# Kernel tuning notes

Hardware: AMD Instinct MI355X
Metric: run time of the kernel (lower is better)

Reference implementation:

```python
import jax, jax.numpy as jnp
import numpy as np

B, N = 1, 1024
C_A, C_Z, H = 768, 128, 16
CH = C_A // H  # 48
INV_SQRT_CH = float(1.0 / np.sqrt(CH))


def _ln(x, w, b):
    # torch.nn.LayerNorm over last dim, eps=1e-5
    m = jnp.mean(x, axis=-1, keepdims=True)
    v = jnp.mean(jnp.square(x - m), axis=-1, keepdims=True)
    return (x - m) * jax.lax.rsqrt(v + 1e-5) * w + b


def setup_inputs() -> dict:
    key = jax.random.key(0)
    ks = jax.random.split(key, 8)
    rn = lambda k, shape, sc: jax.random.normal(k, shape, dtype=jnp.float32) * sc
    return {
        "a": rn(ks[0], (B, N, C_A), 1.0),
        "z": rn(ks[1], (B, N, N, C_Z), 1.0),
        "mask": jnp.ones((B, N), dtype=jnp.float32),
        "ln_a_w": jnp.ones((C_A,), jnp.float32),
        "ln_a_b": jnp.zeros((C_A,), jnp.float32),
        "ln_z_w": jnp.ones((C_Z,), jnp.float32),
        "ln_z_b": jnp.zeros((C_Z,), jnp.float32),
        "Wq": rn(ks[2], (C_A, H * CH), 0.02),
        "bq": jnp.zeros((H * CH,), jnp.float32),
        "Wk": rn(ks[3], (C_A, H * CH), 0.02),
        "Wv": rn(ks[4], (C_A, H * CH), 0.02),
        "Wb": rn(ks[5], (C_Z, H), 0.02),
        "Wg": rn(ks[6], (C_A, H * CH), 0.02),
        "Wo": rn(ks[7], (H * CH, C_A), 0.02),
    }


def reference(a, z, mask, ln_a_w, ln_a_b, ln_z_w, ln_z_b, Wq, bq, Wk, Wv, Wb, Wg, Wo):
    an = _ln(a, ln_a_w, ln_a_b)                                  # [B, N, C_A]
    q = (an @ Wq + bq).reshape(B, N, H, CH)
    k = (an @ Wk).reshape(B, N, H, CH)
    v = (an @ Wv).reshape(B, N, H, CH)
    # pair bias: LayerNorm(z) -> per-head scalar bias [B, N, N, H]
    bpair = _ln(z, ln_z_w, ln_z_b) @ Wb
    mbias = (mask - 1.0)[:, None, None, :] * 1e9                  # [B, 1, 1, N]
    logits = jnp.einsum('bqhc,bkhc->bhqk', q, k) * INV_SQRT_CH
    logits = logits + jnp.transpose(bpair, (0, 3, 1, 2)) + mbias  # [B, H, N, N]
    attn = jax.nn.softmax(logits, axis=-1)
    o = jnp.einsum('bhqk,bkhc->bqhc', attn, v)                    # [B, N, H, CH]
    g = jax.nn.sigmoid(an @ Wg).reshape(B, N, H, CH)
    out = (g * o).reshape(B, N, H * CH) @ Wo                      # [B, N, C_A]
    return out
```

## Files before the change

### kernel.cpp

```cpp
#include <hip/hip_runtime.h>

#define NSEQ 1024
#define CA   768
#define CZ   128
#define NH   16
#define CHD  48
#define HC   768
#define INV_SQRT_CH 0.14433756729740643f

typedef float v4f __attribute__((ext_vector_type(4)));
typedef short v8s __attribute__((ext_vector_type(8)));

__device__ __forceinline__ short f2bf(float f) {
  union { float f; unsigned u; } v; v.f = f;
  unsigned r = v.u + 0x7fffu + ((v.u >> 16) & 1u);
  return (short)(r >> 16);
}
__device__ __forceinline__ float bf2f(short s) {
  union { unsigned u; float f; } v;
  v.u = ((unsigned)(unsigned short)s) << 16;
  return v.f;
}
__device__ __forceinline__ unsigned cvtpk(float lo, float hi) {
  unsigned r;
  asm("v_cvt_pk_bf16_f32 %0, %1, %2" : "=v"(r) : "v"(lo), "v"(hi));
  return r;
}

__global__ __launch_bounds__(256) void k_front(
    const float* __restrict__ lnzw, const float* __restrict__ lnzb,
    const float* __restrict__ Wb, short* __restrict__ wWp, float* __restrict__ S1bW,
    const float* __restrict__ Wq, const float* __restrict__ Wk,
    const float* __restrict__ Wv, const float* __restrict__ Wg,
    const float* __restrict__ Wo, short* __restrict__ WT, short* __restrict__ WoT,
    const float* __restrict__ a, const float* __restrict__ lnaw,
    const float* __restrict__ lnab, short* __restrict__ anb)
{
  __shared__ __align__(16) char fsm[64 * 65 * 4];
  const int bid = blockIdx.x;
  const int t = threadIdx.x;

  if (bid == 0) {
    const int s = t >> 6, l = t & 63;
    const int r16 = l & 15, cg = l >> 4;
    float v[8];
    #pragma unroll
    for (int j = 0; j < 8; ++j) {
      int d = s * 32 + cg * 8 + j;
      v[j] = lnzw[d] * Wb[d * NH + r16];
    }
    uint4 pk;
    pk.x = cvtpk(v[0], v[1]); pk.y = cvtpk(v[2], v[3]);
    pk.z = cvtpk(v[4], v[5]); pk.w = cvtpk(v[6], v[7]);
    *(uint4*)(wWp + (s * 64 + l) * 8) = pk;
    if (t < NH) {
      float s1 = 0.f, bw = 0.f;
      for (int d = 0; d < CZ; ++d) {
        float wb = Wb[d * NH + t];
        s1 += bf2f(f2bf(lnzw[d] * wb));
        bw += lnzb[d] * wb;
      }
      S1bW[t] = s1;
      S1bW[NH + t] = bw;
    }
  } else if (bid <= 720) {
    float (*tile)[65] = (float(*)[65])fsm;
    const int cb = bid - 1;
    const int mat = cb / 144, rem = cb % 144;
    const int tk = rem % 12, tn = rem / 12;
    const int k0 = tk * 64, n0 = tn * 64;
    const float* __restrict__ W =
        (mat == 0) ? Wq : (mat == 1) ? Wk : (mat == 2) ? Wv : (mat == 3) ? Wg : Wo;
    const float s = (mat == 0) ? INV_SQRT_CH : 1.f;
    const int rr = t >> 4, cc = (t & 15) * 4;
    #pragma unroll
    for (int r = 0; r < 4; ++r) {
      v4f v = *(const v4f*)(W + (size_t)(k0 + r * 16 + rr) * HC + n0 + cc);
      tile[r * 16 + rr][cc + 0] = v[0];
      tile[r * 16 + rr][cc + 1] = v[1];
      tile[r * 16 + rr][cc + 2] = v[2];
      tile[r * 16 + rr][cc + 3] = v[3];
    }
    __syncthreads();
    short* dst = (mat < 4) ? (WT + (size_t)mat * HC * CA) : WoT;
    #pragma unroll
    for (int r = 0; r < 4; ++r) {
      const int nr = r * 16 + rr;
      uint2 pk;
      pk.x = cvtpk(tile[cc + 0][nr] * s, tile[cc + 1][nr] * s);
      pk.y = cvtpk(tile[cc + 2][nr] * s, tile[cc + 3][nr] * s);
      *(uint2*)(dst + (size_t)(n0 + nr) * CA + k0 + cc) = pk;
    }
  } else {
    float* red = (float*)fsm;
    const int row = bid - 721;
    const float* ar = a + (size_t)row * CA;
    float x[3];
    float s = 0.f, s2 = 0.f;
    #pragma unroll
    for (int i = 0; i < 3; ++i) {
      x[i] = ar[t + i * 256];
      s += x[i]; s2 += x[i] * x[i];
    }
    #pragma unroll
    for (int off = 1; off < 64; off <<= 1) {
      s += __shfl_xor(s, off);
      s2 += __shfl_xor(s2, off);
    }
    const int wv = t >> 6;
    if ((t & 63) == 0) { red[wv] = s; red[4 + wv] = s2; }
    __syncthreads();
    s = red[0] + red[1] + red[2] + red[3];
    s2 = red[4] + red[5] + red[6] + red[7];
    const float m = s * (1.f / CA);
    const float var = s2 * (1.f / CA) - m * m;
    const float rs = rsqrtf(var + 1e-5f);
    #pragma unroll
    for (int i = 0; i < 3; ++i) {
      int c = t + i * 256;
      anb[(size_t)row * CA + c] = f2bf((x[i] - m) * rs * lnaw[c] + lnab[c]);
    }
  }
}

__global__ __launch_bounds__(256) void k23_mega(
    const short* __restrict__ anb, const short* __restrict__ WT,
    const float* __restrict__ bq, const float* __restrict__ z,
    const short* __restrict__ wWp, const float* __restrict__ S1bW,
    short* __restrict__ qb, short* __restrict__ kb, short* __restrict__ vT,
    float* __restrict__ gbuf, short* __restrict__ bpair)
{
  __shared__ __align__(16) char smem[20480];
  const int tid = threadIdx.x;
  const int w = tid >> 6, l = tid & 63;
  const int r16 = l & 15, cg = l >> 4;

  if (blockIdx.x < 192) {
    short* As = (short*)smem;
    short* Bs = (short*)(smem + 10240);
    const int bm = blockIdx.x & 7;
    const int bnb = blockIdx.x >> 3;
    const int m0 = bm * 128, n0 = bnb * 128;
    const int wr = w >> 1, wc = w & 1;
    const int strow = w * 16 + (l >> 2);
    const int scol = (l & 3) * 8;

    v4f acc[4][4];
    #pragma unroll
    for (int i = 0; i < 4; ++i)
      #pragma unroll
      for (int j = 0; j < 4; ++j)
        acc[i][j] = (v4f){0.f, 0.f, 0.f, 0.f};

    for (int k0 = 0; k0 < CA; k0 += 32) {
      v8s av0 = *(const v8s*)(anb + (size_t)(m0 + strow) * CA + k0 + scol);
      v8s av1 = *(const v8s*)(anb + (size_t)(m0 + 64 + strow) * CA + k0 + scol);
      v8s bv0 = *(const v8s*)(WT + (size_t)(n0 + strow) * CA + k0 + scol);
      v8s bv1 = *(const v8s*)(WT + (size_t)(n0 + 64 + strow) * CA + k0 + scol);
      __syncthreads();
      *(v8s*)(As + (size_t)strow * 40 + scol) = av0;
      *(v8s*)(As + (size_t)(64 + strow) * 40 + scol) = av1;
      *(v8s*)(Bs + (size_t)strow * 40 + scol) = bv0;
      *(v8s*)(Bs + (size_t)(64 + strow) * 40 + scol) = bv1;
      __syncthreads();
      v8s a[4], b[4];
      #pragma unroll
      for (int m = 0; m < 4; ++m)
        a[m] = *(const v8s*)(As + (wr * 64 + m * 16 + r16) * 40 + cg * 8);
      #pragma unroll
      for (int n = 0; n < 4; ++n)
        b[n] = *(const v8s*)(Bs + (wc * 64 + n * 16 + r16) * 40 + cg * 8);
      #pragma unroll
      for (int m = 0; m < 4; ++m)
        #pragma unroll
        for (int n = 0; n < 4; ++n)
          acc[m][n] = __builtin_amdgcn_mfma_f32_16x16x32_bf16(a[m], b[n], acc[m][n], 0, 0, 0);
    }

    const int matsel = n0 / HC;
    #pragma unroll
    for (int n = 0; n < 4; ++n) {
      const int nc = (n0 % HC) + wc * 64 + n * 16 + r16;
      const int rbase = m0 + wr * 64 + cg * 4;
      if (matsel == 0) {
        const float bqs = bq[nc] * INV_SQRT_CH;
        #pragma unroll
        for (int m = 0; m < 4; ++m)
          #pragma unroll
          for (int j = 0; j < 4; ++j)
            qb[(size_t)(rbase + m * 16 + j) * HC + nc] = f2bf(acc[m][n][j] + bqs);
      } else if (matsel == 1) {
        #pragma unroll
        for (int m = 0; m < 4; ++m)
          #pragma unroll
          for (int j = 0; j < 4; ++j)
            kb[(size_t)(rbase + m * 16 + j) * HC + nc] = f2bf(acc[m][n][j]);
      } else if (matsel == 2) {
        #pragma unroll
        for (int m = 0; m < 4; ++m) {
          uint2 pk;
          pk.x = cvtpk(acc[m][n][0], acc[m][n][1]);
          pk.y = cvtpk(acc[m][n][2], acc[m][n][3]);
          *(uint2*)(vT + (size_t)nc * NSEQ + rbase + m * 16) = pk;
        }
      } else {
        #pragma unroll
        for (int m = 0; m < 4; ++m)
          #pragma unroll
          for (int j = 0; j < 4; ++j)
            gbuf[(size_t)(rbase + m * 16 + j) * HC + nc] =
                1.f / (1.f + __expf(-acc[m][n][j]));
      }
    }
  } else {
    const int zbid = blockIdx.x - 192;
    short* bl = (short*)smem + w * (16 * 68);
    const int q = zbid >> 2;
    const int kw = ((zbid & 3) << 8) + w * 64;

    v8s bfrag[4];
    #pragma unroll
    for (int s = 0; s < 4; ++s) bfrag[s] = *(const v8s*)(wWp + (s * 64 + l) * 8);
    const float S1 = S1bW[r16];
    const float bW = S1bW[NH + r16];

    const float* __restrict__ zbase = z + ((size_t)q * NSEQ + kw + r16) * CZ;

    v4f zb[8];
    #pragma unroll
    for (int s = 0; s < 4; ++s) {
      zb[2 * s]     = *(const v4f*)(zbase + s * 32 + cg * 8);
      zb[2 * s + 1] = *(const v4f*)(zbase + s * 32 + cg * 8 + 4);
    }

    for (int kt = 0; kt < 4; ++kt) {
      v4f zn[8];
      if (kt < 3) {
        const float* __restrict__ zr2 = zbase + (size_t)(kt + 1) * 16 * CZ;
        #pragma unroll
        for (int s = 0; s < 4; ++s) {
          zn[2 * s]     = *(const v4f*)(zr2 + s * 32 + cg * 8);
          zn[2 * s + 1] = *(const v4f*)(zr2 + s * 32 + cg * 8 + 4);
        }
      }

      float sum = 0.f, sum2 = 0.f;
      v8s afrag[4];
      #pragma unroll
      for (int s = 0; s < 4; ++s) {
        v4f z0 = zb[2 * s], z1 = zb[2 * s + 1];
        #pragma unroll
        for (int j = 0; j < 4; ++j) {
          sum += z0[j] + z1[j];
          sum2 += z0[j] * z0[j] + z1[j] * z1[j];
        }
        union { v8s s8; unsigned u[4]; } fu;
        fu.u[0] = cvtpk(z0[0], z0[1]);
        fu.u[1] = cvtpk(z0[2], z0[3]);
        fu.u[2] = cvtpk(z1[0], z1[1]);
        fu.u[3] = cvtpk(z1[2], z1[3]);
        afrag[s] = fu.s8;
      }
      sum  += __shfl_xor(sum, 16);  sum  += __shfl_xor(sum, 32);
      sum2 += __shfl_xor(sum2, 16); sum2 += __shfl_xor(sum2, 32);
      const float mean = sum * (1.f / CZ);
      const float var = sum2 * (1.f / CZ) - mean * mean;
      const float rs = rsqrtf(var + 1e-5f);

      v4f acc = {0.f, 0.f, 0.f, 0.f};
      #pragma unroll
      for (int s = 0; s < 4; ++s)
        acc = __builtin_amdgcn_mfma_f32_16x16x32_bf16(afrag[s], bfrag[s], acc, 0, 0, 0);

      float bv[4];
      #pragma unroll
      for (int j = 0; j < 4; ++j) {
        int src = cg * 4 + j;
        float mj = __shfl(mean, src);
        float rj = __shfl(rs, src);
        bv[j] = rj * (acc[j] - mj * S1) + bW;
      }
      *(unsigned*)&bl[r16 * 68 + kt * 16 + cg * 4]     = cvtpk(bv[0], bv[1]);
      *(unsigned*)&bl[r16 * 68 + kt * 16 + cg * 4 + 2] = cvtpk(bv[2], bv[3]);

      if (kt < 3) {
        #pragma unroll
        for (int i = 0; i < 8; ++i) zb[i] = zn[i];
      }
    }

    asm volatile("s_waitcnt lgkmcnt(0)" ::: "memory");
    __builtin_amdgcn_sched_barrier(0);

    const int h = l >> 2, ck = (l & 3) * 16;
    v8s o0 = *(const v8s*)(bl + h * 68 + ck);
    v8s o1 = *(const v8s*)(bl + h * 68 + ck + 8);
    short* dst = bpair + (size_t)h * NSEQ * NSEQ + (size_t)q * NSEQ + kw + ck;
    *(v8s*)(dst)     = o0;
    *(v8s*)(dst + 8) = o1;
  }
}

#define PL_STRIDE 136
#define PO_STRIDE 52
__global__ __launch_bounds__(512) void k45_attn(
    const short* __restrict__ qb, const short* __restrict__ kb,
    const short* __restrict__ vT, const short* __restrict__ bpair,
    const float* __restrict__ mask, const float* __restrict__ gbuf,
    short* __restrict__ gob)
{
  const int h = blockIdx.x & 15;
  const int qt = blockIdx.x >> 4;
  const int tid = threadIdx.x;
  const int w = tid >> 6, l = tid & 63;
  const int r16 = l & 15, cg = l >> 4;
  const int q0 = qt * 16;
  const int k0 = w * 128;

  __shared__ __align__(16) short plds[8][16 * PL_STRIDE];
  __shared__ __align__(16) float po_lds[8][16][PO_STRIDE];
  __shared__ __align__(16) float ml_lds[8][16][2];
  short* pl = &plds[w][0];

  const v8s vzero = {0, 0, 0, 0, 0, 0, 0, 0};
  v8s qf0, qf1;
  {
    const short* qp = qb + (size_t)(q0 + r16) * HC + h * CHD;
    qf0 = *(const v8s*)(qp + cg * 8);
    qf1 = (cg < 2) ? *(const v8s*)(qp + 32 + cg * 8) : vzero;
  }

  const size_t bpb = (size_t)h * NSEQ * NSEQ;
  {
    const int srow = l >> 2;
    const int scol = (l & 3) * 32;
    const short* bsrc = bpair + bpb + (size_t)(q0 + srow) * NSEQ + k0 + scol;
    short* bdst = pl + srow * PL_STRIDE + scol;
    v8s t0 = *(const v8s*)(bsrc);
    v8s t1 = *(const v8s*)(bsrc + 8);
    v8s t2 = *(const v8s*)(bsrc + 16);
    v8s t3 = *(const v8s*)(bsrc + 24);
    *(v8s*)(bdst)      = t0;
    *(v8s*)(bdst + 8)  = t1;
    *(v8s*)(bdst + 16) = t2;
    *(v8s*)(bdst + 24) = t3;
  }

  v4f cs[8];
  #pragma unroll
  for (int kt = 0; kt < 8; ++kt) {
    const short* kp = kb + (size_t)(k0 + kt * 16 + r16) * HC + h * CHD;
    v8s b0 = *(const v8s*)(kp + cg * 8);
    v8s b1 = (cg < 2) ? *(const v8s*)(kp + 32 + cg * 8) : vzero;
    v4f tacc = {0.f, 0.f, 0.f, 0.f};
    tacc = __builtin_amdgcn_mfma_f32_16x16x32_bf16(qf0, b0, tacc, 0, 0, 0);
    tacc = __builtin_amdgcn_mfma_f32_16x16x32_bf16(qf1, b1, tacc, 0, 0, 0);
    cs[kt] = tacc;
  }

  #pragma unroll
  for (int kt = 0; kt < 8; ++kt) {
    const int kc = k0 + kt * 16 + r16;
    const float mb = (mask[kc] - 1.f) * 1e9f;
    #pragma unroll
    for (int j = 0; j < 4; ++j)
      cs[kt][j] += bf2f(pl[(cg * 4 + j) * PL_STRIDE + kt * 16 + r16]) + mb;
  }

  float mx4[4], ls4[4];
  #pragma unroll
  for (int j = 0; j < 4; ++j) {
    float mx = fmaxf(fmaxf(fmaxf(cs[0][j], cs[1][j]), fmaxf(cs[2][j], cs[3][j])),
                     fmaxf(fmaxf(cs[4][j], cs[5][j]), fmaxf(cs[6][j], cs[7][j])));
    mx = fmaxf(mx, __shfl_xor(mx, 1));
    mx = fmaxf(mx, __shfl_xor(mx, 2));
    mx = fmaxf(mx, __shfl_xor(mx, 4));
    mx = fmaxf(mx, __shfl_xor(mx, 8));
    mx4[j] = mx;
    float p[8];
    #pragma unroll
    for (int kt = 0; kt < 8; ++kt) p[kt] = __expf(cs[kt][j] - mx);
    float rsum = ((p[0] + p[1]) + (p[2] + p[3])) + ((p[4] + p[5]) + (p[6] + p[7]));
    rsum += __shfl_xor(rsum, 1);
    rsum += __shfl_xor(rsum, 2);
    rsum += __shfl_xor(rsum, 4);
    rsum += __shfl_xor(rsum, 8);
    ls4[j] = rsum;
    const int rowb = (cg * 4 + j) * PL_STRIDE;
    #pragma unroll
    for (int t2 = 0; t2 < 4; ++t2) {
      unsigned u = cvtpk(p[2 * t2], p[2 * t2 + 1]);
      pl[rowb + (2 * t2) * 16 + r16] = (short)u;
      pl[rowb + (2 * t2 + 1) * 16 + r16] = (short)(u >> 16);
    }
  }
  asm volatile("s_waitcnt lgkmcnt(0)" ::: "memory");
  __builtin_amdgcn_sched_barrier(0);

  v4f of0 = {0, 0, 0, 0}, of1 = {0, 0, 0, 0}, of2 = {0, 0, 0, 0};
  #pragma unroll
  for (int ks4 = 0; ks4 < 4; ++ks4) {
    v8s pa = *(const v8s*)(pl + r16 * PL_STRIDE + ks4 * 32 + cg * 8);
    const short* vp = vT + (size_t)(h * CHD + r16) * NSEQ + k0 + ks4 * 32 + cg * 8;
    v8s bv0 = *(const v8s*)vp;
    v8s bv1 = *(const v8s*)(vp + 16 * NSEQ);
    v8s bv2 = *(const v8s*)(vp + 32 * NSEQ);
    of0 = __builtin_amdgcn_mfma_f32_16x16x32_bf16(pa, bv0, of0, 0, 0, 0);
    of1 = __builtin_amdgcn_mfma_f32_16x16x32_bf16(pa, bv1, of1, 0, 0, 0);
    of2 = __builtin_amdgcn_mfma_f32_16x16x32_bf16(pa, bv2, of2, 0, 0, 0);
  }

  #pragma unroll
  for (int j = 0; j < 4; ++j) {
    const int row = cg * 4 + j;
    po_lds[w][row][r16]      = of0[j];
    po_lds[w][row][16 + r16] = of1[j];
    po_lds[w][row][32 + r16] = of2[j];
    if (r16 == 0) {
      ml_lds[w][row][0] = mx4[j];
      ml_lds[w][row][1] = ls4[j];
    }
  }
  __syncthreads();

  {
    const int g = tid >> 5;
    const int lane = tid & 31;
    float mi[8], li[8];
    #pragma unroll
    for (int i = 0; i < 8; ++i) {
      mi[i] = ml_lds[i][g][0];
      li[i] = ml_lds[i][g][1];
    }
    float mstar = -1e30f;
    #pragma unroll
    for (int i = 0; i < 8; ++i) mstar = fmaxf(mstar, mi[i]);
    float wgt[8], L = 0.f;
    #pragma unroll
    for (int i = 0; i < 8; ++i) { wgt[i] = __expf(mi[i] - mstar); L += li[i] * wgt[i]; }
    const float inv = 1.f / L;
    const int q = q0 + g;
    {
      float o = 0.f;
      #pragma unroll
      for (int i = 0; i < 8; ++i) o += po_lds[i][g][lane] * wgt[i];
      const float gv = gbuf[(size_t)q * HC + h * CHD + lane];
      gob[(size_t)q * HC + h * CHD + lane] = f2bf(o * inv * gv);
    }
    if (lane < 16) {
      const int d = 32 + lane;
      float o = 0.f;
      #pragma unroll
      for (int i = 0; i < 8; ++i) o += po_lds[i][g][d] * wgt[i];
      const float gv = gbuf[(size_t)q * HC + h * CHD + d];
      gob[(size_t)q * HC + h * CHD + d] = f2bf(o * inv * gv);
    }
  }
}

__global__ __launch_bounds__(256) void k5_out(
    const short* __restrict__ gob, const short* __restrict__ WoT,
    float* __restrict__ out)
{
  __shared__ __align__(16) short As[64 * 40];
  __shared__ __align__(16) short Bs[64 * 40];
  const int tid = threadIdx.x;
  const int w = tid >> 6, l = tid & 63;
  const int r16 = l & 15, cg = l >> 4;
  const int bm = blockIdx.x & 15;
  const int bn = blockIdx.x >> 4;
  const int m0 = bm * 64, n0 = bn * 64;
  const int wr = w >> 1, wc = w & 1;
  const int strow = tid >> 2;
  const int scol = (tid & 3) * 8;

  v4f acc[2][2];
  #pragma unroll
  for (int i = 0; i < 2; ++i)
    #pragma unroll
    for (int j = 0; j < 2; ++j)
      acc[i][j] = (v4f){0.f, 0.f, 0.f, 0.f};

  for (int k0 = 0; k0 < CA; k0 += 32) {
    v8s av = *(const v8s*)(gob + (size_t)(m0 + strow) * CA + k0 + scol);
    v8s bv = *(const v8s*)(WoT + (size_t)(n0 + strow) * CA + k0 + scol);
    __syncthreads();
    *(v8s*)(As + (size_t)strow * 40 + scol) = av;
    *(v8s*)(Bs + (size_t)strow * 40 + scol) = bv;
    __syncthreads();
    v8s a[2], b[2];
    #pragma unroll
    for (int m = 0; m < 2; ++m)
      a[m] = *(const v8s*)(As + (wr * 32 + m * 16 + r16) * 40 + cg * 8);
    #pragma unroll
    for (int n = 0; n < 2; ++n)
      b[n] = *(const v8s*)(Bs + (wc * 32 + n * 16 + r16) * 40 + cg * 8);
    #pragma unroll
    for (int m = 0; m < 2; ++m)
      #pragma unroll
      for (int n = 0; n < 2; ++n)
        acc[m][n] = __builtin_amdgcn_mfma_f32_16x16x32_bf16(a[m], b[n], acc[m][n], 0, 0, 0);
  }

  #pragma unroll
  for (int n = 0; n < 2; ++n) {
    const int nc = n0 + wc * 32 + n * 16 + r16;
    const int rbase = m0 + wr * 32 + cg * 4;
    #pragma unroll
    for (int m = 0; m < 2; ++m)
      #pragma unroll
      for (int j = 0; j < 4; ++j)
        out[(size_t)(rbase + m * 16 + j) * CA + nc] = acc[m][n][j];
  }
}

extern "C" void kernel_launch(void* const* d_in, const int* in_sizes, int n_in,
                              void* d_out, int out_size, void* d_ws, size_t ws_size,
                              hipStream_t stream) {
  const float* a      = (const float*)d_in[0];
  const float* z      = (const float*)d_in[1];
  const float* mask   = (const float*)d_in[2];
  const float* ln_a_w = (const float*)d_in[3];
  const float* ln_a_b = (const float*)d_in[4];
  const float* ln_z_w = (const float*)d_in[5];
  const float* ln_z_b = (const float*)d_in[6];
  const float* Wq     = (const float*)d_in[7];
  const float* bq     = (const float*)d_in[8];
  const float* Wk     = (const float*)d_in[9];
  const float* Wv     = (const float*)d_in[10];
  const float* Wb     = (const float*)d_in[11];
  const float* Wg     = (const float*)d_in[12];
  const float* Wo     = (const float*)d_in[13];
  float* out = (float*)d_out;

  char* ws = (char*)d_ws;
  short* anb   = (short*)(ws);
  short* WT    = (short*)(ws + (2ull << 20));
  short* WoT   = (short*)(ws + (7ull << 20));
  short* qb    = (short*)(ws + (9ull << 20));
  short* kb    = (short*)(ws + (11ull << 20));
  short* vT    = (short*)(ws + (13ull << 20));
  float* gbuf  = (float*)(ws + (15ull << 20));
  short* wWp   = (short*)(ws + (19ull << 20));
  float* S1bW  = (float*)(ws + (19ull << 20) + 4096ull);
  short* gob   = (short*)(ws + (20ull << 20));
  short* bpair = (short*)(ws + (22ull << 20));

  k_front<<<1745, 256, 0, stream>>>(ln_z_w, ln_z_b, Wb, wWp, S1bW,
                                    Wq, Wk, Wv, Wg, Wo, WT, WoT,
                                    a, ln_a_w, ln_a_b, anb);
  k23_mega<<<192 + 4096, 256, 0, stream>>>(anb, WT, bq, z, wWp, S1bW,
                                           qb, kb, vT, gbuf, bpair);
  k45_attn<<<1024, 512, 0, stream>>>(qb, kb, vT, bpair, mask, gbuf, gob);
  k5_out<<<192, 256, 0, stream>>>(gob, WoT, out);
}
```

Measured before the change: 173.1 us.

## Fold front prep kernel into consumers: inline LayerNorm and weight transpose

Removes the k_front kernel. LayerNorm of `a`, the fp32-to-bf16 weight transpose, and the pair-bias weight preparation now run inside the GEMM, pair-bias and output kernels. This drops one launch and the round trip of the intermediate bf16 buffers. In exchange, every GEMM tile recomputes row stats and re-converts the weights it needs, and it reads W with strided scalar loads (8 per thread per k-step, with poor coalescing). Redundant LN and weight work is also repeated across the 24 column blocks and the 4096 bias blocks.

```diff
diff --git a/kernel.cpp b/kernel.cpp
--- a/kernel.cpp
+++ b/kernel.cpp
@@ -27,110 +27,18 @@
   return r;
 }
 
-__global__ __launch_bounds__(256) void k_front(
-    const float* __restrict__ lnzw, const float* __restrict__ lnzb,
-    const float* __restrict__ Wb, short* __restrict__ wWp, float* __restrict__ S1bW,
+__global__ __launch_bounds__(256, 2) void k23_mega(
+    const float* __restrict__ a, const float* __restrict__ lnaw,
+    const float* __restrict__ lnab,
     const float* __restrict__ Wq, const float* __restrict__ Wk,
     const float* __restrict__ Wv, const float* __restrict__ Wg,
-    const float* __restrict__ Wo, short* __restrict__ WT, short* __restrict__ WoT,
-    const float* __restrict__ a, const float* __restrict__ lnaw,
-    const float* __restrict__ lnab, short* __restrict__ anb)
-{
-  __shared__ __align__(16) char fsm[64 * 65 * 4];
-  const int bid = blockIdx.x;
-  const int t = threadIdx.x;
-
-  if (bid == 0) {
-    const int s = t >> 6, l = t & 63;
-    const int r16 = l & 15, cg = l >> 4;
-    float v[8];
-    #pragma unroll
-    for (int j = 0; j < 8; ++j) {
-      int d = s * 32 + cg * 8 + j;
-      v[j] = lnzw[d] * Wb[d * NH + r16];
-    }
-    uint4 pk;
-    pk.x = cvtpk(v[0], v[1]); pk.y = cvtpk(v[2], v[3]);
-    pk.z = cvtpk(v[4], v[5]); pk.w = cvtpk(v[6], v[7]);
-    *(uint4*)(wWp + (s * 64 + l) * 8) = pk;
-    if (t < NH) {
-      float s1 = 0.f, bw = 0.f;
-      for (int d = 0; d < CZ; ++d) {
-        float wb = Wb[d * NH + t];
-        s1 += bf2f(f2bf(lnzw[d] * wb));
-        bw += lnzb[d] * wb;
-      }
-      S1bW[t] = s1;
-      S1bW[NH + t] = bw;
-    }
-  } else if (bid <= 720) {
-    float (*tile)[65] = (float(*)[65])fsm;
-    const int cb = bid - 1;
-    const int mat = cb / 144, rem = cb % 144;
-    const int tk = rem % 12, tn = rem / 12;
-    const int k0 = tk * 64, n0 = tn * 64;
-    const float* __restrict__ W =
-        (mat == 0) ? Wq : (mat == 1) ? Wk : (mat == 2) ? Wv : (mat == 3) ? Wg : Wo;
-    const float s = (mat == 0) ? INV_SQRT_CH : 1.f;
-    const int rr = t >> 4, cc = (t & 15) * 4;
-    #pragma unroll
-    for (int r = 0; r < 4; ++r) {
-      v4f v = *(const v4f*)(W + (size_t)(k0 + r * 16 + rr) * HC + n0 + cc);
-      tile[r * 16 + rr][cc + 0] = v[0];
-      tile[r * 16 + rr][cc + 1] = v[1];
-      tile[r * 16 + rr][cc + 2] = v[2];
-      tile[r * 16 + rr][cc + 3] = v[3];
-    }
-    __syncthreads();
-    short* dst = (mat < 4) ? (WT + (size_t)mat * HC * CA) : WoT;
-    #pragma unroll
-    for (int r = 0; r < 4; ++r) {
-      const int nr = r * 16 + rr;
-      uint2 pk;
-      pk.x = cvtpk(tile[cc + 0][nr] * s, tile[cc + 1][nr] * s);
-      pk.y = cvtpk(tile[cc + 2][nr] * s, tile[cc + 3][nr] * s);
-      *(uint2*)(dst + (size_t)(n0 + nr) * CA + k0 + cc) = pk;
-    }
-  } else {
-    float* red = (float*)fsm;
-    const int row = bid - 721;
-    const float* ar = a + (size_t)row * CA;
-    float x[3];
-    float s = 0.f, s2 = 0.f;
-    #pragma unroll
-    for (int i = 0; i < 3; ++i) {
-      x[i] = ar[t + i * 256];
-      s += x[i]; s2 += x[i] * x[i];
-    }
-    #pragma unroll
-    for (int off = 1; off < 64; off <<= 1) {
-      s += __shfl_xor(s, off);
-      s2 += __shfl_xor(s2, off);
-    }
-    const int wv = t >> 6;
-    if ((t & 63) == 0) { red[wv] = s; red[4 + wv] = s2; }
-    __syncthreads();
-    s = red[0] + red[1] + red[2] + red[3];
-    s2 = red[4] + red[5] + red[6] + red[7];
-    const float m = s * (1.f / CA);
-    const float var = s2 * (1.f / CA) - m * m;
-    const float rs = rsqrtf(var + 1e-5f);
-    #pragma unroll
-    for (int i = 0; i < 3; ++i) {
-      int c = t + i * 256;
-      anb[(size_t)row * CA + c] = f2bf((x[i] - m) * rs * lnaw[c] + lnab[c]);
-    }
-  }
-}
-
-__global__ __launch_bounds__(256) void k23_mega(
-    const short* __restrict__ anb, const short* __restrict__ WT,
     const float* __restrict__ bq, const float* __restrict__ z,
-    const short* __restrict__ wWp, const float* __restrict__ S1bW,
+    const float* __restrict__ lnzw, const float* __restrict__ lnzb,
+    const float* __restrict__ Wb,
     short* __restrict__ qb, short* __restrict__ kb, short* __restrict__ vT,
     float* __restrict__ gbuf, short* __restrict__ bpair)
 {
-  __shared__ __align__(16) char smem[20480];
+  __shared__ __align__(16) char smem[21504];
   const int tid = threadIdx.x;
   const int w = tid >> 6, l = tid & 63;
   const int r16 = l & 15, cg = l >> 4;
@@ -138,13 +46,42 @@
   if (blockIdx.x < 192) {
     short* As = (short*)smem;
     short* Bs = (short*)(smem + 10240);
+    float* stats = (float*)(smem + 20480);
     const int bm = blockIdx.x & 7;
     const int bnb = blockIdx.x >> 3;
     const int m0 = bm * 128, n0 = bnb * 128;
+    const int matsel = n0 / HC;
+    const float* __restrict__ Wsrc =
+        (matsel == 0) ? Wq : (matsel == 1) ? Wk : (matsel == 2) ? Wv : Wg;
+    const float wscale = (matsel == 0) ? INV_SQRT_CH : 1.f;
     const int wr = w >> 1, wc = w & 1;
     const int strow = w * 16 + (l >> 2);
     const int scol = (l & 3) * 8;
 
+    {
+      const int row = tid >> 1, half = tid & 1;
+      const float* ar = a + (size_t)(m0 + row) * CA + half * 384;
+      float s = 0.f, s2 = 0.f;
+      for (int i = 0; i < 96; ++i) {
+        v4f x = *(const v4f*)(ar + i * 4);
+        s += (x[0] + x[1]) + (x[2] + x[3]);
+        s2 += (x[0] * x[0] + x[1] * x[1]) + (x[2] * x[2] + x[3] * x[3]);
+      }
+      s += __shfl_xor(s, 1);
+      s2 += __shfl_xor(s2, 1);
+      if (half == 0) {
+        const float m = s * (1.f / CA);
+        const float var = s2 * (1.f / CA) - m * m;
+        stats[row * 2] = m;
+        stats[row * 2 + 1] = rsqrtf(var + 1e-5f);
+      }
+    }
+    __syncthreads();
+
+    const float mA0 = stats[strow * 2],        rA0 = stats[strow * 2 + 1];
+    const float mA1 = stats[(64 + strow) * 2], rA1 = stats[(64 + strow) * 2 + 1];
+    const int ncb = (n0 % HC) + strow;
+
     v4f acc[4][4];
     #pragma unroll
     for (int i = 0; i < 4; ++i)
@@ -153,31 +90,53 @@
         acc[i][j] = (v4f){0.f, 0.f, 0.f, 0.f};
 
     for (int k0 = 0; k0 < CA; k0 += 32) {
-      v8s av0 = *(const v8s*)(anb + (size_t)(m0 + strow) * CA + k0 + scol);
-      v8s av1 = *(const v8s*)(anb + (size_t)(m0 + 64 + strow) * CA + k0 + scol);
-      v8s bv0 = *(const v8s*)(WT + (size_t)(n0 + strow) * CA + k0 + scol);
-      v8s bv1 = *(const v8s*)(WT + (size_t)(n0 + 64 + strow) * CA + k0 + scol);
+      v4f x0 = *(const v4f*)(a + (size_t)(m0 + strow) * CA + k0 + scol);
+      v4f x1 = *(const v4f*)(a + (size_t)(m0 + strow) * CA + k0 + scol + 4);
+      v4f y0 = *(const v4f*)(a + (size_t)(m0 + 64 + strow) * CA + k0 + scol);
+      v4f y1 = *(const v4f*)(a + (size_t)(m0 + 64 + strow) * CA + k0 + scol + 4);
+      v4f lw0 = *(const v4f*)(lnaw + k0 + scol);
+      v4f lw1 = *(const v4f*)(lnaw + k0 + scol + 4);
+      v4f lb0 = *(const v4f*)(lnab + k0 + scol);
+      v4f lb1 = *(const v4f*)(lnab + k0 + scol + 4);
+      float b0f[8], b1f[8];
+      #pragma unroll
+      for (int j = 0; j < 8; ++j) {
+        b0f[j] = Wsrc[(size_t)(k0 + scol + j) * HC + ncb] * wscale;
+        b1f[j] = Wsrc[(size_t)(k0 + scol + j) * HC + ncb + 64] * wscale;
+      }
+      uint4 pa0, pa1, pb0, pb1;
+      pa0.x = cvtpk((x0[0]-mA0)*rA0*lw0[0]+lb0[0], (x0[1]-mA0)*rA0*lw0[1]+lb0[1]);
+      pa0.y = cvtpk((x0[2]-mA0)*rA0*lw0[2]+lb0[2], (x0[3]-mA0)*rA0*lw0[3]+lb0[3]);
+      pa0.z = cvtpk((x1[0]-mA0)*rA0*lw1[0]+lb1[0], (x1[1]-mA0)*rA0*lw1[1]+lb1[1]);
+      pa0.w = cvtpk((x1[2]-mA0)*rA0*lw1[2]+lb1[2], (x1[3]-mA0)*rA0*lw1[3]+lb1[3]);
+      pa1.x = cvtpk((y0[0]-mA1)*rA1*lw0[0]+lb0[0], (y0[1]-mA1)*rA1*lw0[1]+lb0[1]);
+      pa1.y = cvtpk((y0[2]-mA1)*rA1*lw0[2]+lb0[2], (y0[3]-mA1)*rA1*lw0[3]+lb0[3]);
+      pa1.z = cvtpk((y1[0]-mA1)*rA1*lw1[0]+lb1[0], (y1[1]-mA1)*rA1*lw1[1]+lb1[1]);
+      pa1.w = cvtpk((y1[2]-mA1)*rA1*lw1[2]+lb1[2], (y1[3]-mA1)*rA1*lw1[3]+lb1[3]);
+      pb0.x = cvtpk(b0f[0], b0f[1]); pb0.y = cvtpk(b0f[2], b0f[3]);
+      pb0.z = cvtpk(b0f[4], b0f[5]); pb0.w = cvtpk(b0f[6], b0f[7]);
+      pb1.x = cvtpk(b1f[0], b1f[1]); pb1.y = cvtpk(b1f[2], b1f[3]);
+      pb1.z = cvtpk(b1f[4], b1f[5]); pb1.w = cvtpk(b1f[6], b1f[7]);
       __syncthreads();
-      *(v8s*)(As + (size_t)strow * 40 + scol) = av0;
-      *(v8s*)(As + (size_t)(64 + strow) * 40 + scol) = av1;
-      *(v8s*)(Bs + (size_t)strow * 40 + scol) = bv0;
-      *(v8s*)(Bs + (size_t)(64 + strow) * 40 + scol) = bv1;
+      *(uint4*)(As + (size_t)strow * 40 + scol) = pa0;
+      *(uint4*)(As + (size_t)(64 + strow) * 40 + scol) = pa1;
+      *(uint4*)(Bs + (size_t)strow * 40 + scol) = pb0;
+      *(uint4*)(Bs + (size_t)(64 + strow) * 40 + scol) = pb1;
       __syncthreads();
-      v8s a[4], b[4];
+      v8s af[4], bf[4];
       #pragma unroll
       for (int m = 0; m < 4; ++m)
-        a[m] = *(const v8s*)(As + (wr * 64 + m * 16 + r16) * 40 + cg * 8);
+        af[m] = *(const v8s*)(As + (wr * 64 + m * 16 + r16) * 40 + cg * 8);
       #pragma unroll
       for (int n = 0; n < 4; ++n)
-        b[n] = *(const v8s*)(Bs + (wc * 64 + n * 16 + r16) * 40 + cg * 8);
+        bf[n] = *(const v8s*)(Bs + (wc * 64 + n * 16 + r16) * 40 + cg * 8);
       #pragma unroll
       for (int m = 0; m < 4; ++m)
         #pragma unroll
         for (int n = 0; n < 4; ++n)
-          acc[m][n] = __builtin_amdgcn_mfma_f32_16x16x32_bf16(a[m], b[n], acc[m][n], 0, 0, 0);
-    }
-
-    const int matsel = n0 / HC;
+          acc[m][n] = __builtin_amdgcn_mfma_f32_16x16x32_bf16(af[m], bf[n], acc[m][n], 0, 0, 0);
+    }
+
     #pragma unroll
     for (int n = 0; n < 4; ++n) {
       const int nc = (n0 % HC) + wc * 64 + n * 16 + r16;
@@ -219,18 +178,37 @@
     const int kw = ((zbid & 3) << 8) + w * 64;
 
     v8s bfrag[4];
-    #pragma unroll
-    for (int s = 0; s < 4; ++s) bfrag[s] = *(const v8s*)(wWp + (s * 64 + l) * 8);
-    const float S1 = S1bW[r16];
-    const float bW = S1bW[NH + r16];
+    float s1 = 0.f, bwp = 0.f;
+    #pragma unroll
+    for (int ss = 0; ss < 4; ++ss) {
+      unsigned up[4];
+      #pragma unroll
+      for (int jj = 0; jj < 4; ++jj) {
+        const int d0 = ss * 32 + cg * 8 + jj * 2;
+        const float wb0 = Wb[d0 * NH + r16];
+        const float wb1 = Wb[(d0 + 1) * NH + r16];
+        const short c0 = f2bf(lnzw[d0] * wb0);
+        const short c1 = f2bf(lnzw[d0 + 1] * wb1);
+        s1 += bf2f(c0) + bf2f(c1);
+        bwp += lnzb[d0] * wb0 + lnzb[d0 + 1] * wb1;
+        up[jj] = (unsigned)(unsigned short)c0 | ((unsigned)(unsigned short)c1 << 16);
+      }
+      union { v8s s8; unsigned u[4]; } fu;
+      fu.u[0] = up[0]; fu.u[1] = up[1]; fu.u[2] = up[2]; fu.u[3] = up[3];
+      bfrag[ss] = fu.s8;
+    }
+    s1  += __shfl_xor(s1, 16);  s1  += __shfl_xor(s1, 32);
+    bwp += __shfl_xor(bwp, 16); bwp += __shfl_xor(bwp, 32);
+    const float S1 = s1;
+    const float bW = bwp;
 
     const float* __restrict__ zbase = z + ((size_t)q * NSEQ + kw + r16) * CZ;
 
     v4f zb[8];
     #pragma unroll
-    for (int s = 0; s < 4; ++s) {
-      zb[2 * s]     = *(const v4f*)(zbase + s * 32 + cg * 8);
-      zb[2 * s + 1] = *(const v4f*)(zbase + s * 32 + cg * 8 + 4);
+    for (int ss = 0; ss < 4; ++ss) {
+      zb[2 * ss]     = *(const v4f*)(zbase + ss * 32 + cg * 8);
+      zb[2 * ss + 1] = *(const v4f*)(zbase + ss * 32 + cg * 8 + 4);
     }
 
     for (int kt = 0; kt < 4; ++kt) {
@@ -238,17 +216,17 @@
       if (kt < 3) {
         const float* __restrict__ zr2 = zbase + (size_t)(kt + 1) * 16 * CZ;
         #pragma unroll
-        for (int s = 0; s < 4; ++s) {
-          zn[2 * s]     = *(const v4f*)(zr2 + s * 32 + cg * 8);
-          zn[2 * s + 1] = *(const v4f*)(zr2 + s * 32 + cg * 8 + 4);
+        for (int ss = 0; ss < 4; ++ss) {
+          zn[2 * ss]     = *(const v4f*)(zr2 + ss * 32 + cg * 8);
+          zn[2 * ss + 1] = *(const v4f*)(zr2 + ss * 32 + cg * 8 + 4);
         }
       }
 
       float sum = 0.f, sum2 = 0.f;
       v8s afrag[4];
       #pragma unroll
-      for (int s = 0; s < 4; ++s) {
-        v4f z0 = zb[2 * s], z1 = zb[2 * s + 1];
+      for (int ss = 0; ss < 4; ++ss) {
+        v4f z0 = zb[2 * ss], z1 = zb[2 * ss + 1];
         #pragma unroll
         for (int j = 0; j < 4; ++j) {
           sum += z0[j] + z1[j];
@@ -259,7 +237,7 @@
         fu.u[1] = cvtpk(z0[2], z0[3]);
         fu.u[2] = cvtpk(z1[0], z1[1]);
         fu.u[3] = cvtpk(z1[2], z1[3]);
-        afrag[s] = fu.s8;
+        afrag[ss] = fu.s8;
       }
       sum  += __shfl_xor(sum, 16);  sum  += __shfl_xor(sum, 32);
       sum2 += __shfl_xor(sum2, 16); sum2 += __shfl_xor(sum2, 32);
@@ -269,8 +247,8 @@
 
       v4f acc = {0.f, 0.f, 0.f, 0.f};
       #pragma unroll
-      for (int s = 0; s < 4; ++s)
-        acc = __builtin_amdgcn_mfma_f32_16x16x32_bf16(afrag[s], bfrag[s], acc, 0, 0, 0);
+      for (int ss = 0; ss < 4; ++ss)
+        acc = __builtin_amdgcn_mfma_f32_16x16x32_bf16(afrag[ss], bfrag[ss], acc, 0, 0, 0);
 
       float bv[4];
       #pragma unroll
@@ -459,7 +437,7 @@
 }
 
 __global__ __launch_bounds__(256) void k5_out(
-    const short* __restrict__ gob, const short* __restrict__ WoT,
+    const short* __restrict__ gob, const float* __restrict__ Wo,
     float* __restrict__ out)
 {
   __shared__ __align__(16) short As[64 * 40];
@@ -473,6 +451,8 @@
   const int wr = w >> 1, wc = w & 1;
   const int strow = tid >> 2;
   const int scol = (tid & 3) * 8;
+  const int kr = tid & 31;
+  const int nb = (tid >> 5) * 8;
 
   v4f acc[2][2];
   #pragma unroll
@@ -483,23 +463,27 @@
 
   for (int k0 = 0; k0 < CA; k0 += 32) {
     v8s av = *(const v8s*)(gob + (size_t)(m0 + strow) * CA + k0 + scol);
-    v8s bv = *(const v8s*)(WoT + (size_t)(n0 + strow) * CA + k0 + scol);
+    v4f w0 = *(const v4f*)(Wo + (size_t)(k0 + kr) * HC + n0 + nb);
+    v4f w1 = *(const v4f*)(Wo + (size_t)(k0 + kr) * HC + n0 + nb + 4);
     __syncthreads();
     *(v8s*)(As + (size_t)strow * 40 + scol) = av;
-    *(v8s*)(Bs + (size_t)strow * 40 + scol) = bv;
+    #pragma unroll
+    for (int i = 0; i < 4; ++i) Bs[(nb + i) * 40 + kr] = f2bf(w0[i]);
+    #pragma unroll
+    for (int i = 0; i < 4; ++i) Bs[(nb + 4 + i) * 40 + kr] = f2bf(w1[i]);
     __syncthreads();
-    v8s a[2], b[2];
+    v8s af[2], bf[2];
     #pragma unroll
     for (int m = 0; m < 2; ++m)
-      a[m] = *(const v8s*)(As + (wr * 32 + m * 16 + r16) * 40 + cg * 8);
+      af[m] = *(const v8s*)(As + (wr * 32 + m * 16 + r16) * 40 + cg * 8);
     #pragma unroll
     for (int n = 0; n < 2; ++n)
-      b[n] = *(const v8s*)(Bs + (wc * 32 + n * 16 + r16) * 40 + cg * 8);
+      bf[n] = *(const v8s*)(Bs + (wc * 32 + n * 16 + r16) * 40 + cg * 8);
     #pragma unroll
     for (int m = 0; m < 2; ++m)
       #pragma unroll
       for (int n = 0; n < 2; ++n)
-        acc[m][n] = __builtin_amdgcn_mfma_f32_16x16x32_bf16(a[m], b[n], acc[m][n], 0, 0, 0);
+        acc[m][n] = __builtin_amdgcn_mfma_f32_16x16x32_bf16(af[m], bf[n], acc[m][n], 0, 0, 0);
   }
 
   #pragma unroll
@@ -534,23 +518,16 @@
   float* out = (float*)d_out;
 
   char* ws = (char*)d_ws;
-  short* anb   = (short*)(ws);
-  short* WT    = (short*)(ws + (2ull << 20));
-  short* WoT   = (short*)(ws + (7ull << 20));
-  short* qb    = (short*)(ws + (9ull << 20));
-  short* kb    = (short*)(ws + (11ull << 20));
-  short* vT    = (short*)(ws + (13ull << 20));
-  float* gbuf  = (float*)(ws + (15ull << 20));
-  short* wWp   = (short*)(ws + (19ull << 20));
-  float* S1bW  = (float*)(ws + (19ull << 20) + 4096ull);
-  short* gob   = (short*)(ws + (20ull << 20));
-  short* bpair = (short*)(ws + (22ull << 20));
-
-  k_front<<<1745, 256, 0, stream>>>(ln_z_w, ln_z_b, Wb, wWp, S1bW,
-                                    Wq, Wk, Wv, Wg, Wo, WT, WoT,
-                                    a, ln_a_w, ln_a_b, anb);
-  k23_mega<<<192 + 4096, 256, 0, stream>>>(anb, WT, bq, z, wWp, S1bW,
+  short* qb    = (short*)(ws);
+  short* kb    = (short*)(ws + (2ull << 20));
+  short* vT    = (short*)(ws + (4ull << 20));
+  float* gbuf  = (float*)(ws + (6ull << 20));
+  short* gob   = (short*)(ws + (10ull << 20));
+  short* bpair = (short*)(ws + (12ull << 20));
+
+  k23_mega<<<192 + 4096, 256, 0, stream>>>(a, ln_a_w, ln_a_b, Wq, Wk, Wv, Wg,
+                                           bq, z, ln_z_w, ln_z_b, Wb,
                                            qb, kb, vT, gbuf, bpair);
   k45_attn<<<1024, 512, 0, stream>>>(qb, kb, vT, bpair, mask, gbuf, gob);
-  k5_out<<<192, 256, 0, stream>>>(gob, WoT, out);
-}
+  k5_out<<<192, 256, 0, stream>>>(gob, Wo, out);
+}
```

Measured after the change: 190.1 us. 1.1x slower.
